# Optimization experiments

Measured on AMD Instinct MI355X. Metric: run time of the kernel, lower is better.

## Reference

```python
import jax, jax.numpy as jnp
import numpy as np

# ---- constant kernels (kornia canny defaults) ----

def _gauss_kernel1d(ksize=5, sigma=1.0):
    x = np.arange(ksize, dtype=np.float32) - (ksize - 1) / 2.0
    g = np.exp(-(x ** 2) / (2.0 * sigma ** 2))
    return (g / g.sum()).astype(np.float32)

_GK = _gauss_kernel1d()
_SOBEL_X = np.array([[-1, 0, 1], [-2, 0, 2], [-1, 0, 1]], np.float32) / 8.0  # normalized=True
_SOBEL_Y = _SOBEL_X.T.copy()

# 8 directional NMS kernels: +1 at center, -1 at neighbor d*45 degrees (kornia order)
_NMS = np.zeros((8, 1, 3, 3), np.float32)
_OFFS = [(0, 1), (1, 1), (1, 0), (1, -1), (0, -1), (-1, -1), (-1, 0), (-1, 1)]
for _i, (_dy, _dx) in enumerate(_OFFS):
    _NMS[_i, 0, 1, 1] = 1.0
    _NMS[_i, 0, 1 + _dy, 1 + _dx] = -1.0


def _conv(x, k):
    return jax.lax.conv_general_dilated(
        x, k, (1, 1), 'VALID', dimension_numbers=('NCHW', 'OIHW', 'NCHW'))


def _canny_dilate(x):
    # x: [B,3,H,W] BGR in [0,1]
    x = x[:, ::-1]  # bgr -> rgb
    gray = 0.299 * x[:, 0:1] + 0.587 * x[:, 1:2] + 0.114 * x[:, 2:3]  # [B,1,H,W]

    # gaussian blur 5x5, sigma=1, reflect padding (separable)
    p = jnp.pad(gray, ((0, 0), (0, 0), (2, 2), (2, 2)), mode='reflect')
    kh = jnp.asarray(_GK).reshape(1, 1, 1, 5)
    kv = jnp.asarray(_GK).reshape(1, 1, 5, 1)
    blurred = _conv(_conv(p, kh), kv)

    # sobel gradients, replicate padding
    sp = jnp.pad(blurred, ((0, 0), (0, 0), (1, 1), (1, 1)), mode='edge')
    sob = jnp.asarray(np.stack([_SOBEL_X, _SOBEL_Y])[:, None])  # (2,1,3,3)
    g = _conv(sp, sob)
    gx, gy = g[:, 0:1], g[:, 1:2]

    mag = jnp.sqrt(gx * gx + gy * gy + 1e-6)  # [B,1,H,W]
    ang45 = jnp.round(jnp.arctan2(gy, gx) * (180.0 / np.pi) / 45.0)  # multiples of 45 deg
    pos_idx = jnp.mod(ang45, 8).astype(jnp.int32)
    neg_idx = jnp.mod(ang45 + 4, 8).astype(jnp.int32)

    # direction-dependent non-maximum suppression
    nms = _conv(jnp.pad(mag, ((0, 0), (0, 0), (1, 1), (1, 1))), jnp.asarray(_NMS))  # [B,8,H,W]
    pos = jnp.take_along_axis(nms, pos_idx, axis=1)
    neg = jnp.take_along_axis(nms, neg_idx, axis=1)
    is_max = jnp.minimum(pos, neg) > 0.0
    mag = mag * is_max

    # morphological dilation, 5x5 ones kernel, geodesic border (pad with -max_val)
    MAX_VAL = 1e4
    padded = jnp.pad(mag, ((0, 0), (0, 0), (2, 2), (2, 2)), constant_values=-MAX_VAL)
    out = jax.lax.reduce_window(padded, -jnp.inf, jax.lax.max,
                                (1, 1, 5, 5), (1, 1, 1, 1), 'VALID')
    return out


def setup_inputs() -> dict:
    key = jax.random.key(0)
    x = jax.random.uniform(key, (32, 3, 512, 512), dtype=jnp.float32)
    return {'x': x}


def reference(x):
    return _canny_dilate(x)
```

## Files before the change

### kernel.cpp

```cpp
#include <hip/hip_runtime.h>
#include <math.h>

#define IMW 512
#define SEG 32
#define NSEG (512/SEG)
#define NSTRIP 10
#define OUTW 52

__device__ __forceinline__ int reflect512(int i) {
    int a = i < 0 ? -i : i;
    int b = 1022 - a;
    return a < b ? a : b;
}
__device__ __forceinline__ float bperm(int a4, float v) {
    return __int_as_float(__builtin_amdgcn_ds_bpermute(a4, __float_as_int(v)));
}

__global__ __launch_bounds__(256)
void canny_pipe(const float* __restrict__ x, float* __restrict__ out) {
    const int lane  = threadIdx.x & 63;
    const int unit  = __builtin_amdgcn_readfirstlane(
                          (int)(blockIdx.x * 4 + (threadIdx.x >> 6)));
    const int img   = unit / (NSTRIP * NSEG);
    const int rem   = unit - img * (NSTRIP * NSEG);
    const int strip = rem / NSEG;
    const int seg   = rem - strip * NSEG;
    const int Y0 = seg * SEG, Y1 = Y0 + SEG;
    const int x0 = strip * OUTW - 6;
    const int xv = x0 + lane;
    const int xr = reflect512(xv);
    const bool inimg  = (xv >= 0) && (xv < IMW);
    const bool stlane = (lane >= 6) && (lane < 58) && (xv < IMW);
    const int l4  = lane << 2;
    const int aL4 = (min(max(xv - 1, 0), 511) - x0) << 2;
    const int aR4 = (min(max(xv + 1, 0), 511) - x0) << 2;

    const float* base = x + (size_t)img * 3 * IMW * IMW;
    const int r0 = reflect512(Y0 - 6);
    const float* b0 = base + (size_t)r0 * IMW;
    const float* b1 = b0 + (size_t)IMW * IMW;
    const float* b2 = b0 + (size_t)2 * IMW * IMW;
    float* ob = out + (size_t)img * IMW * IMW;

    const float K0 = 0.054488684549643f, K1 = 0.244201342003233f, K2 = 0.402619946931554f;

    float hb0=0,hb1=0,hb2=0,hb3=0,hb4=0;
    float hx0=0,hx1=0,hx2=0, hy0=0,hy1=0,hy2=0;
    float mg0=0,mg1=0,mg2=0;
    int   ax0=0, ax1=0;
    float cm0=0,cm1=0,cm2=0,cm3=0,cm4=0;

    float p0 = b0[xr];
    float p1 = b1[xr];
    float p2 = b2[xr];

    #pragma unroll 4
    for (int v = Y0 - 6; v <= Y1 + 5; ++v) {
        float gray = 0.299f * p2 + 0.587f * p1 + 0.114f * p0;
        const int d = ((unsigned)v <= 510u) ? IMW : -IMW;
        b0 += d; b1 += d; b2 += d;
        p0 = b0[xr];
        p1 = b1[xr];
        p2 = b2[xr];

        float gl1 = bperm(l4 - 4, gray), gl2 = bperm(l4 - 8, gray);
        float gr1 = bperm(l4 + 4, gray), gr2 = bperm(l4 + 8, gray);
        hb0 = hb1; hb1 = hb2; hb2 = hb3; hb3 = hb4;
        hb4 = K0 * (gl2 + gr2) + K1 * (gl1 + gr1) + K2 * gray;

        float blur = K0 * (hb0 + hb4) + K1 * (hb1 + hb3) + K2 * hb2;
        float bl = bperm(aL4, blur), br = bperm(aR4, blur);
        hx0 = hx1; hx1 = hx2; hx2 = br - bl;
        hy0 = hy1; hy1 = hy2; hy2 = bl + 2.f * blur + br;

        const int g = v - 3;
        float hxa = (g == 0)   ? hx1 : hx0;
        float hxc = (g == 511) ? hx1 : hx2;
        float hya = (g == 0)   ? hy1 : hy0;
        float hyc = (g == 511) ? hy1 : hy2;
        float gxv = (hxa + 2.f * hx1 + hxc) * 0.125f;
        float gyv = (hyc - hya) * 0.125f;
        float mag = sqrtf(gxv * gxv + gyv * gyv + 1e-6f);
        float axm = fabsf(gxv), aym = fabsf(gyv);
        int axis;
        if (aym <= 0.41421356237309515f * axm)      axis = 0;
        else if (aym >= 2.4142135623730951f * axm)  axis = 2;
        else axis = ((gxv >= 0.f) == (gyv >= 0.f)) ? 1 : 3;
        mg0 = mg1; mg1 = mg2; mg2 = inimg ? mag : 0.f;
        ax0 = ax1; ax1 = axis;

        const int m = v - 4;
        float magm = (m == 0)   ? 0.f : mg0;
        float magc = mg1;
        float magp = (m == 511) ? 0.f : mg2;
        float gcp = bperm(l4 + 4, magc), gcm = bperm(l4 - 4, magc);
        float gpp = bperm(l4 + 4, magp), gpm = bperm(l4 - 4, magp);
        float gmm = bperm(l4 - 4, magm), gmp = bperm(l4 + 4, magm);
        const int dd = ax0;
        float mp = (dd == 0) ? gcp : (dd == 1) ? gpp : (dd == 2) ? magp : gpm;
        float mn = (dd == 0) ? gcm : (dd == 1) ? gmm : (dd == 2) ? magm : gmp;
        float msk = (inimg && fminf(magc - mp, magc - mn) > 0.f) ? magc : 0.f;

        float s1 = fmaxf(bperm(l4 - 4, msk), bperm(l4 + 4, msk));
        float s2 = fmaxf(bperm(l4 - 8, msk), bperm(l4 + 8, msk));
        cm0 = cm1; cm1 = cm2; cm2 = cm3; cm3 = cm4;
        cm4 = fmaxf(fmaxf(s1, s2), msk);

        const int y = v - 6;
        if (y >= Y0) {
            float c0 = (y >= 2)   ? cm0 : 0.f;
            float c1 = (y >= 1)   ? cm1 : 0.f;
            float c3 = (y <= 510) ? cm3 : 0.f;
            float c4 = (y <= 509) ? cm4 : 0.f;
            float val = fmaxf(fmaxf(fmaxf(c0, c1), fmaxf(cm2, c3)), c4);
            if (stlane) ob[(size_t)y * IMW + xv] = val;
        }
    }
}

extern "C" void kernel_launch(void* const* d_in, const int* in_sizes, int n_in,
                              void* d_out, int out_size, void* d_ws, size_t ws_size,
                              hipStream_t stream) {
    const float* x = (const float*)d_in[0];
    float* out = (float*)d_out;
    const int units = 32 * NSTRIP * NSEG;
    dim3 grid(units / 4);
    canny_pipe<<<grid, 256, 0, stream>>>(x, out);
}
```

Before: 175.7 us.

## Process two columns per lane and software-pipeline cross-lane permutes

Each lane now handles two adjacent pixels, so a wavefront covers a 116-column strip instead of 52. This cuts the redundant halo columns and halves the number of ds_bpermute exchanges per pixel. The permute results are staggered across loop iterations, with extra pipeline delay rows, so their latency overlaps with other work. Stores become float2. The cost is more live registers and a longer warm-up per segment.

```diff
diff --git a/kernel.cpp b/kernel.cpp
--- a/kernel.cpp
+++ b/kernel.cpp
@@ -4,8 +4,8 @@
 #define IMW 512
 #define SEG 32
 #define NSEG (512/SEG)
-#define NSTRIP 10
-#define OUTW 52
+#define NSTRIP 5
+#define OUTW 116
 
 __device__ __forceinline__ int reflect512(int i) {
     int a = i < 0 ? -i : i;
@@ -16,104 +16,162 @@
     return __int_as_float(__builtin_amdgcn_ds_bpermute(a4, __float_as_int(v)));
 }
 
-__global__ __launch_bounds__(256)
-void canny_pipe(const float* __restrict__ x, float* __restrict__ out) {
-    const int lane  = threadIdx.x & 63;
-    const int unit  = __builtin_amdgcn_readfirstlane(
-                          (int)(blockIdx.x * 4 + (threadIdx.x >> 6)));
+__global__ __launch_bounds__(128)
+void canny_pipe2(const float* __restrict__ x, float* __restrict__ out) {
+    const int lane = threadIdx.x & 63;
+    const int unit = __builtin_amdgcn_readfirstlane(
+                         (int)(blockIdx.x * 2 + (threadIdx.x >> 6)));
     const int img   = unit / (NSTRIP * NSEG);
     const int rem   = unit - img * (NSTRIP * NSEG);
     const int strip = rem / NSEG;
     const int seg   = rem - strip * NSEG;
     const int Y0 = seg * SEG, Y1 = Y0 + SEG;
-    const int x0 = strip * OUTW - 6;
-    const int xv = x0 + lane;
-    const int xr = reflect512(xv);
-    const bool inimg  = (xv >= 0) && (xv < IMW);
-    const bool stlane = (lane >= 6) && (lane < 58) && (xv < IMW);
-    const int l4  = lane << 2;
-    const int aL4 = (min(max(xv - 1, 0), 511) - x0) << 2;
-    const int aR4 = (min(max(xv + 1, 0), 511) - x0) << 2;
+    const int xbase = strip * OUTW - 6;
+    const int xa = xbase + 2 * lane, xb = xa + 1;
+    const int xra = reflect512(xa), xrb = reflect512(xb);
+    const bool inA = (xa >= 0) && (xa < IMW);
+    const bool inB = (xb >= 0) && (xb < IMW);
+    const bool stl = (lane >= 3) && (lane < 61) && (xb < IMW);
+    const int lm4 = ((lane - 1) & 63) << 2;
+    const int lp4 = ((lane + 1) & 63) << 2;
+    const bool clampL = (xa == 0);
+    const bool clampR = (xb == IMW - 1);
 
     const float* base = x + (size_t)img * 3 * IMW * IMW;
-    const int r0 = reflect512(Y0 - 6);
-    const float* b0 = base + (size_t)r0 * IMW;
+    const float* b0 = base + (size_t)reflect512(Y0 - 6) * IMW;
     const float* b1 = b0 + (size_t)IMW * IMW;
     const float* b2 = b0 + (size_t)2 * IMW * IMW;
     float* ob = out + (size_t)img * IMW * IMW;
 
     const float K0 = 0.054488684549643f, K1 = 0.244201342003233f, K2 = 0.402619946931554f;
 
-    float hb0=0,hb1=0,hb2=0,hb3=0,hb4=0;
-    float hx0=0,hx1=0,hx2=0, hy0=0,hy1=0,hy2=0;
-    float mg0=0,mg1=0,mg2=0;
-    int   ax0=0, ax1=0;
-    float cm0=0,cm1=0,cm2=0,cm3=0,cm4=0;
+    float h0a=0,h1a=0,h2a=0,h3a=0,h4a=0, h0b=0,h1b=0,h2b=0,h3b=0,h4b=0;
+    float hxA0=0,hxA1=0,hxA2=0, hxB0=0,hxB1=0,hxB2=0;
+    float hyA0=0,hyA1=0,hyA2=0, hyB0=0,hyB1=0,hyB2=0;
+    float mgA0=0,mgA1=0,mgA2=0, mgB0=0,mgB1=0,mgB2=0;
+    float smM0=0,smM1=0,smM2=0, smP0=0,smP1=0,smP2=0;
+    int   axA0=0,axA1=0,axA2=0, axB0=0,axB1=0,axB2=0;
+    float cmA0=0,cmA1=0,cmA2=0,cmA3=0,cmA4=0;
+    float cmB0=0,cmB1=0,cmB2=0,cmB3=0,cmB4=0;
+    float pga=0, pgb=0;
+    float pba=0, pbb=0;
+    float psa=0, psb=0;
+    float qg_am=0, qg_ap=0, qg_bm=0, qg_bp=0;
+    float qb_bm=0, qb_ap=0;
+    float qm_bm=0, qm_ap=0;
+    float qs_am=0, qs_ap=0, qs_bm=0, qs_bp=0;
 
-    float p0 = b0[xr];
-    float p1 = b1[xr];
-    float p2 = b2[xr];
+    float f0a = b0[xra], f0b = b0[xrb];
+    float f1a = b1[xra], f1b = b1[xrb];
+    float f2a = b2[xra], f2b = b2[xrb];
 
     #pragma unroll 4
-    for (int v = Y0 - 6; v <= Y1 + 5; ++v) {
-        float gray = 0.299f * p2 + 0.587f * p1 + 0.114f * p0;
+    for (int v = Y0 - 6; v <= Y1 + 9; ++v) {
+        float ga = 0.299f * f2a + 0.587f * f1a + 0.114f * f0a;
+        float gb = 0.299f * f2b + 0.587f * f1b + 0.114f * f0b;
         const int d = ((unsigned)v <= 510u) ? IMW : -IMW;
         b0 += d; b1 += d; b2 += d;
-        p0 = b0[xr];
-        p1 = b1[xr];
-        p2 = b2[xr];
+        f0a = b0[xra]; f0b = b0[xrb];
+        f1a = b1[xra]; f1b = b1[xrb];
+        f2a = b2[xra]; f2b = b2[xrb];
 
-        float gl1 = bperm(l4 - 4, gray), gl2 = bperm(l4 - 8, gray);
-        float gr1 = bperm(l4 + 4, gray), gr2 = bperm(l4 + 8, gray);
-        hb0 = hb1; hb1 = hb2; hb2 = hb3; hb3 = hb4;
-        hb4 = K0 * (gl2 + gr2) + K1 * (gl1 + gr1) + K2 * gray;
+        float hba = K0 * (qg_am + qg_ap) + K1 * (qg_bm + pgb) + K2 * pga;
+        float hbb = K0 * (qg_bm + qg_bp) + K1 * (pga + qg_ap) + K2 * pgb;
+        pga = ga; pgb = gb;
+        qg_am = bperm(lm4, ga); qg_ap = bperm(lp4, ga);
+        qg_bm = bperm(lm4, gb); qg_bp = bperm(lp4, gb);
+        h0a=h1a; h1a=h2a; h2a=h3a; h3a=h4a; h4a=hba;
+        h0b=h1b; h1b=h2b; h2b=h3b; h3b=h4b; h4b=hbb;
 
-        float blur = K0 * (hb0 + hb4) + K1 * (hb1 + hb3) + K2 * hb2;
-        float bl = bperm(aL4, blur), br = bperm(aR4, blur);
-        hx0 = hx1; hx1 = hx2; hx2 = br - bl;
-        hy0 = hy1; hy1 = hy2; hy2 = bl + 2.f * blur + br;
+        float bla = K0 * (h0a + h4a) + K1 * (h1a + h3a) + K2 * h2a;
+        float blb = K0 * (h0b + h4b) + K1 * (h1b + h3b) + K2 * h2b;
 
-        const int g = v - 3;
-        float hxa = (g == 0)   ? hx1 : hx0;
-        float hxc = (g == 511) ? hx1 : hx2;
-        float hya = (g == 0)   ? hy1 : hy0;
-        float hyc = (g == 511) ? hy1 : hy2;
-        float gxv = (hxa + 2.f * hx1 + hxc) * 0.125f;
-        float gyv = (hyc - hya) * 0.125f;
-        float mag = sqrtf(gxv * gxv + gyv * gyv + 1e-6f);
-        float axm = fabsf(gxv), aym = fabsf(gyv);
-        int axis;
-        if (aym <= 0.41421356237309515f * axm)      axis = 0;
-        else if (aym >= 2.4142135623730951f * axm)  axis = 2;
-        else axis = ((gxv >= 0.f) == (gyv >= 0.f)) ? 1 : 3;
-        mg0 = mg1; mg1 = mg2; mg2 = inimg ? mag : 0.f;
-        ax0 = ax1; ax1 = axis;
+        smM0=smM1; smM1=smM2; smM2=qm_bm;
+        smP0=smP1; smP1=smP2; smP2=qm_ap;
+        {
+            const int m = v - 7;
+            float m0a = (m==0)?0.f:mgA0, m0b = (m==0)?0.f:mgB0;
+            float s0m = (m==0)?0.f:smM0, s0p = (m==0)?0.f:smP0;
+            float m2a = (m==511)?0.f:mgA2, m2b = (m==511)?0.f:mgB2;
+            float s2m = (m==511)?0.f:smM2, s2p = (m==511)?0.f:smP2;
+            const int da = axA1;
+            float mpa = (da==0) ? mgB1 : (da==1) ? m2b : (da==2) ? m2a : s2m;
+            float mna = (da==0) ? smM1 : (da==1) ? s0m : (da==2) ? m0a : m0b;
+            float cena = mgA1;
+            float mska_ = (inA && fminf(cena - mpa, cena - mna) > 0.f) ? cena : 0.f;
+            const int db = axB1;
+            float mpb = (db==0) ? smP1 : (db==1) ? s2p : (db==2) ? m2b : m2a;
+            float mnb = (db==0) ? mgA1 : (db==1) ? m0a : (db==2) ? m0b : s0p;
+            float cenb = mgB1;
+            float mskb_ = (inB && fminf(cenb - mpb, cenb - mnb) > 0.f) ? cenb : 0.f;
 
-        const int m = v - 4;
-        float magm = (m == 0)   ? 0.f : mg0;
-        float magc = mg1;
-        float magp = (m == 511) ? 0.f : mg2;
-        float gcp = bperm(l4 + 4, magc), gcm = bperm(l4 - 4, magc);
-        float gpp = bperm(l4 + 4, magp), gpm = bperm(l4 - 4, magp);
-        float gmm = bperm(l4 - 4, magm), gmp = bperm(l4 + 4, magm);
-        const int dd = ax0;
-        float mp = (dd == 0) ? gcp : (dd == 1) ? gpp : (dd == 2) ? magp : gpm;
-        float mn = (dd == 0) ? gcm : (dd == 1) ? gmm : (dd == 2) ? magm : gmp;
-        float msk = (inimg && fminf(magc - mp, magc - mn) > 0.f) ? magc : 0.f;
+            float cma = fmaxf(fmaxf(qs_am, qs_bm), fmaxf(fmaxf(psa, psb), qs_ap));
+            float cmb = fmaxf(fmaxf(qs_bm, psa), fmaxf(fmaxf(psb, qs_ap), qs_bp));
+            cmA0=cmA1; cmA1=cmA2; cmA2=cmA3; cmA3=cmA4; cmA4=cma;
+            cmB0=cmB1; cmB1=cmB2; cmB2=cmB3; cmB3=cmB4; cmB4=cmb;
+            psa = mska_; psb = mskb_;
+            qs_am = bperm(lm4, mska_); qs_ap = bperm(lp4, mska_);
+            qs_bm = bperm(lm4, mskb_); qs_bp = bperm(lp4, mskb_);
+        }
 
-        float s1 = fmaxf(bperm(l4 - 4, msk), bperm(l4 + 4, msk));
-        float s2 = fmaxf(bperm(l4 - 8, msk), bperm(l4 + 8, msk));
-        cm0 = cm1; cm1 = cm2; cm2 = cm3; cm3 = cm4;
-        cm4 = fmaxf(fmaxf(s1, s2), msk);
+        {
+            float la = clampL ? pba : qb_bm;
+            float ra = pbb;
+            float lb = pba;
+            float rb = clampR ? pbb : qb_ap;
+            float nxa = ra - la, nya = la + 2.f * pba + ra;
+            float nxb = rb - lb, nyb = lb + 2.f * pbb + rb;
+            hxA0=hxA1; hxA1=hxA2; hxA2=nxa;  hxB0=hxB1; hxB1=hxB2; hxB2=nxb;
+            hyA0=hyA1; hyA1=hyA2; hyA2=nya;  hyB0=hyB1; hyB1=hyB2; hyB2=nyb;
+            pba = bla; pbb = blb;
+            qb_bm = bperm(lm4, blb); qb_ap = bperm(lp4, bla);
+        }
 
-        const int y = v - 6;
-        if (y >= Y0) {
-            float c0 = (y >= 2)   ? cm0 : 0.f;
-            float c1 = (y >= 1)   ? cm1 : 0.f;
-            float c3 = (y <= 510) ? cm3 : 0.f;
-            float c4 = (y <= 509) ? cm4 : 0.f;
-            float val = fmaxf(fmaxf(fmaxf(c0, c1), fmaxf(cm2, c3)), c4);
-            if (stlane) ob[(size_t)y * IMW + xv] = val;
+        {
+            const int g = v - 5;
+            float hxaa = (g==0) ? hxA1 : hxA0;  float hxca = (g==511) ? hxA1 : hxA2;
+            float hyaa = (g==0) ? hyA1 : hyA0;  float hyca = (g==511) ? hyA1 : hyA2;
+            float gxa = (hxaa + 2.f * hxA1 + hxca) * 0.125f;
+            float gya = (hyca - hyaa) * 0.125f;
+            float maga = sqrtf(gxa * gxa + gya * gya + 1e-6f);
+            float axma = fabsf(gxa), ayma = fabsf(gya);
+            int aa;
+            if (ayma <= 0.41421356237309515f * axma)      aa = 0;
+            else if (ayma >= 2.4142135623730951f * axma)  aa = 2;
+            else aa = ((gxa >= 0.f) == (gya >= 0.f)) ? 1 : 3;
+
+            float hxab = (g==0) ? hxB1 : hxB0;  float hxcb = (g==511) ? hxB1 : hxB2;
+            float hyab = (g==0) ? hyB1 : hyB0;  float hycb = (g==511) ? hyB1 : hyB2;
+            float gxb = (hxab + 2.f * hxB1 + hxcb) * 0.125f;
+            float gyb = (hycb - hyab) * 0.125f;
+            float magb = sqrtf(gxb * gxb + gyb * gyb + 1e-6f);
+            float axmb = fabsf(gxb), aymb = fabsf(gyb);
+            int ab;
+            if (aymb <= 0.41421356237309515f * axmb)      ab = 0;
+            else if (aymb >= 2.4142135623730951f * axmb)  ab = 2;
+            else ab = ((gxb >= 0.f) == (gyb >= 0.f)) ? 1 : 3;
+
+            mgA0=mgA1; mgA1=mgA2; mgA2 = inA ? maga : 0.f;
+            mgB0=mgB1; mgB1=mgB2; mgB2 = inB ? magb : 0.f;
+            axA0=axA1; axA1=axA2; axA2=aa;
+            axB0=axB1; axB1=axB2; axB2=ab;
+            qm_bm = bperm(lm4, mgB2); qm_ap = bperm(lp4, mgA2);
+        }
+
+        {
+            const int y = v - 10;
+            if (y >= Y0) {
+                float c0a=(y>=2)?cmA0:0.f, c1a=(y>=1)?cmA1:0.f;
+                float c3a=(y<=510)?cmA3:0.f, c4a=(y<=509)?cmA4:0.f;
+                float va = fmaxf(fmaxf(fmaxf(c0a, c1a), fmaxf(cmA2, c3a)), c4a);
+                float c0b=(y>=2)?cmB0:0.f, c1b=(y>=1)?cmB1:0.f;
+                float c3b=(y<=510)?cmB3:0.f, c4b=(y<=509)?cmB4:0.f;
+                float vb = fmaxf(fmaxf(fmaxf(c0b, c1b), fmaxf(cmB2, c3b)), c4b);
+                if (stl) {
+                    float2 t; t.x = va; t.y = vb;
+                    *(float2*)(ob + (size_t)y * IMW + xa) = t;
+                }
+            }
         }
     }
 }
@@ -124,6 +182,6 @@
     const float* x = (const float*)d_in[0];
     float* out = (float*)d_out;
     const int units = 32 * NSTRIP * NSEG;
-    dim3 grid(units / 4);
-    canny_pipe<<<grid, 256, 0, stream>>>(x, out);
+    dim3 grid(units / 2);
+    canny_pipe2<<<grid, 128, 0, stream>>>(x, out);
 }
```

After: 179.4 us. 2.1% more time.

## Process full image rows per wavefront with 8 pixels per lane and DPP shuffles

Applied to the files above, without the earlier changes.

Replaces the 64-wide overlapping column strips (52 useful lanes of 64) with one wavefront covering an entire 512-pixel row, where each lane holds 8 pixels loaded as two float4 vectors. Horizontal neighbour exchange moves from ds_bpermute to DPP row rotates and shifts plus in-register access, and the segment height drops from 32 to 8 rows. Interior segments use a template specialization with no border checks, and the block index is swizzled. This removes the redundant strip-overlap work and the LDS-permute traffic, but the short segments mean 12 warm-up rows per 8 output rows, which adds recomputation and raises register pressure.

```diff
diff --git a/kernel.cpp b/kernel.cpp
--- a/kernel.cpp
+++ b/kernel.cpp
@@ -2,120 +2,303 @@
 #include <math.h>
 
 #define IMW 512
-#define SEG 32
-#define NSEG (512/SEG)
-#define NSTRIP 10
-#define OUTW 52
+#define SEG 8
+#define NSEG 64
+
+template<int CTRL>
+__device__ __forceinline__ float dpp_mov(float v) {
+    return __int_as_float(__builtin_amdgcn_update_dpp(
+        0, __float_as_int(v), CTRL, 0xF, 0xF, true));
+}
+#define ROTR1(v) dpp_mov<0x13C>(v)
+#define SHR1(v)  dpp_mov<0x138>(v)
+#define ROTL1(v) dpp_mov<0x134>(v)
+#define SHL1(v)  dpp_mov<0x130>(v)
 
 __device__ __forceinline__ int reflect512(int i) {
     int a = i < 0 ? -i : i;
     int b = 1022 - a;
     return a < b ? a : b;
 }
-__device__ __forceinline__ float bperm(int a4, float v) {
-    return __int_as_float(__builtin_amdgcn_ds_bpermute(a4, __float_as_int(v)));
-}
-
-__global__ __launch_bounds__(256)
-void canny_pipe(const float* __restrict__ x, float* __restrict__ out) {
-    const int lane  = threadIdx.x & 63;
-    const int unit  = __builtin_amdgcn_readfirstlane(
-                          (int)(blockIdx.x * 4 + (threadIdx.x >> 6)));
-    const int img   = unit / (NSTRIP * NSEG);
-    const int rem   = unit - img * (NSTRIP * NSEG);
-    const int strip = rem / NSEG;
-    const int seg   = rem - strip * NSEG;
+
+struct CT { static constexpr bool value = true;  };
+struct CF { static constexpr bool value = false; };
+
+template<bool EDGE>
+__device__ __forceinline__ void run_rows(
+    const float* b0, const float* b1, const float* b2, float* ob,
+    const int Y0, const int Y1, const int lane)
+{
+    const float K0 = 0.054488684549643f, K1 = 0.244201342003233f,
+                K2 = 0.402619946931554f;
+    const bool l0  = (lane == 0);
+    const bool l63 = (lane == 63);
+    const int  vo  = lane * 4;
+
+    float hb[5][8];
+    float hx[3][8], hy[3][8];
+    float mg[3][8];
+    int   ax[2][8];
+    float cm[5][8];
+    #pragma unroll
+    for (int r = 0; r < 5; ++r) {
+        #pragma unroll
+        for (int e = 0; e < 8; ++e) { hb[r][e] = 0.f; cm[r][e] = 0.f; }
+    }
+    #pragma unroll
+    for (int r = 0; r < 3; ++r) {
+        #pragma unroll
+        for (int e = 0; e < 8; ++e) { hx[r][e] = 0.f; hy[r][e] = 0.f; mg[r][e] = 0.f; }
+    }
+    #pragma unroll
+    for (int r = 0; r < 2; ++r) {
+        #pragma unroll
+        for (int e = 0; e < 8; ++e) ax[r][e] = 0;
+    }
+
+    float4 c0A = *(const float4*)(b0 + vo), c0B = *(const float4*)(b0 + 256 + vo);
+    float4 c1A = *(const float4*)(b1 + vo), c1B = *(const float4*)(b1 + 256 + vo);
+    float4 c2A = *(const float4*)(b2 + vo), c2B = *(const float4*)(b2 + 256 + vo);
+
+    auto iter = [&](int v, auto st) {
+        constexpr bool STORE = decltype(st)::value;
+
+        float gA[4] = {
+            0.299f*c2A.x + 0.587f*c1A.x + 0.114f*c0A.x,
+            0.299f*c2A.y + 0.587f*c1A.y + 0.114f*c0A.y,
+            0.299f*c2A.z + 0.587f*c1A.z + 0.114f*c0A.z,
+            0.299f*c2A.w + 0.587f*c1A.w + 0.114f*c0A.w };
+        float gB[4] = {
+            0.299f*c2B.x + 0.587f*c1B.x + 0.114f*c0B.x,
+            0.299f*c2B.y + 0.587f*c1B.y + 0.114f*c0B.y,
+            0.299f*c2B.z + 0.587f*c1B.z + 0.114f*c0B.z,
+            0.299f*c2B.w + 0.587f*c1B.w + 0.114f*c0B.w };
+
+        {
+            int d;
+            if constexpr (EDGE) d = ((unsigned)v <= 510u) ? IMW : -IMW;
+            else                d = IMW;
+            b0 += d; b1 += d; b2 += d;
+        }
+        c0A = *(const float4*)(b0 + vo); c0B = *(const float4*)(b0 + 256 + vo);
+        c1A = *(const float4*)(b1 + vo); c1B = *(const float4*)(b1 + 256 + vo);
+        c2A = *(const float4*)(b2 + vo); c2B = *(const float4*)(b2 + 256 + vo);
+
+        {
+            float rAe2 = ROTR1(gA[2]), rAe3 = ROTR1(gA[3]);
+            float rBe2 = ROTR1(gB[2]), rBe3 = ROTR1(gB[3]);
+            float lAe0 = ROTL1(gA[0]), lAe1 = ROTL1(gA[1]);
+            float lBe0 = ROTL1(gB[0]), lBe1 = ROTL1(gB[1]);
+            float Am1 = l0  ? gA[1] : rAe3;
+            float Am2 = l0  ? gA[2] : rAe2;
+            float Bm1 = l0  ? rAe3  : rBe3;
+            float Bm2 = l0  ? rAe2  : rBe2;
+            float Ap1 = l63 ? lBe0  : lAe0;
+            float Ap2 = l63 ? lBe1  : lAe1;
+            float Bp1 = l63 ? gB[2] : lBe0;
+            float Bp2 = l63 ? gB[1] : lBe1;
+            float nh[8] = {
+                K0*(Am2  +gA[2]) + K1*(Am1  +gA[1]) + K2*gA[0],
+                K0*(Am1  +gA[3]) + K1*(gA[0]+gA[2]) + K2*gA[1],
+                K0*(gA[0]+Ap1  ) + K1*(gA[1]+gA[3]) + K2*gA[2],
+                K0*(gA[1]+Ap2  ) + K1*(gA[2]+Ap1  ) + K2*gA[3],
+                K0*(Bm2  +gB[2]) + K1*(Bm1  +gB[1]) + K2*gB[0],
+                K0*(Bm1  +gB[3]) + K1*(gB[0]+gB[2]) + K2*gB[1],
+                K0*(gB[0]+Bp1  ) + K1*(gB[1]+gB[3]) + K2*gB[2],
+                K0*(gB[1]+Bp2  ) + K1*(gB[2]+Bp1  ) + K2*gB[3] };
+            #pragma unroll
+            for (int r = 0; r < 4; ++r) {
+                #pragma unroll
+                for (int e = 0; e < 8; ++e) hb[r][e] = hb[r+1][e];
+            }
+            #pragma unroll
+            for (int e = 0; e < 8; ++e) hb[4][e] = nh[e];
+        }
+
+        {
+            float bl[8];
+            #pragma unroll
+            for (int e = 0; e < 8; ++e)
+                bl[e] = K0*(hb[0][e]+hb[4][e]) + K1*(hb[1][e]+hb[3][e]) + K2*hb[2][e];
+            float rA3 = ROTR1(bl[3]), rB3 = ROTR1(bl[7]);
+            float lA0 = ROTL1(bl[0]), lB0 = ROTL1(bl[4]);
+            float sAm1 = l0  ? bl[0] : rA3;
+            float sBm1 = l0  ? rA3   : rB3;
+            float sAp1 = l63 ? lB0   : lA0;
+            float sBp1 = l63 ? bl[7] : lB0;
+            float nx[8] = { bl[1]-sAm1, bl[2]-bl[0], bl[3]-bl[1], sAp1-bl[2],
+                            bl[5]-sBm1, bl[6]-bl[4], bl[7]-bl[5], sBp1-bl[6] };
+            float ny[8] = { sAm1+2.f*bl[0]+bl[1], bl[0]+2.f*bl[1]+bl[2],
+                            bl[1]+2.f*bl[2]+bl[3], bl[2]+2.f*bl[3]+sAp1,
+                            sBm1+2.f*bl[4]+bl[5], bl[4]+2.f*bl[5]+bl[6],
+                            bl[5]+2.f*bl[6]+bl[7], bl[6]+2.f*bl[7]+sBp1 };
+            #pragma unroll
+            for (int r = 0; r < 2; ++r) {
+                #pragma unroll
+                for (int e = 0; e < 8; ++e) { hx[r][e] = hx[r+1][e]; hy[r][e] = hy[r+1][e]; }
+            }
+            #pragma unroll
+            for (int e = 0; e < 8; ++e) { hx[2][e] = nx[e]; hy[2][e] = ny[e]; }
+        }
+
+        {
+            const int g = v - 3;
+            float nmg[8]; int nax[8];
+            #pragma unroll
+            for (int e = 0; e < 8; ++e) {
+                float hxa, hxc, hya, hyc;
+                if constexpr (EDGE) {
+                    hxa = (g==0)   ? hx[1][e] : hx[0][e];
+                    hxc = (g==511) ? hx[1][e] : hx[2][e];
+                    hya = (g==0)   ? hy[1][e] : hy[0][e];
+                    hyc = (g==511) ? hy[1][e] : hy[2][e];
+                } else {
+                    hxa = hx[0][e]; hxc = hx[2][e]; hya = hy[0][e]; hyc = hy[2][e];
+                }
+                float gx = (hxa + 2.f*hx[1][e] + hxc) * 0.125f;
+                float gy = (hyc - hya) * 0.125f;
+                float mag = sqrtf(gx*gx + gy*gy + 1e-6f);
+                float axm = fabsf(gx), aym = fabsf(gy);
+                int a;
+                if (aym <= 0.41421356237309515f * axm)      a = 0;
+                else if (aym >= 2.4142135623730951f * axm)  a = 2;
+                else a = ((gx >= 0.f) == (gy >= 0.f)) ? 1 : 3;
+                nmg[e] = mag; nax[e] = a;
+            }
+            #pragma unroll
+            for (int r = 0; r < 2; ++r) {
+                #pragma unroll
+                for (int e = 0; e < 8; ++e) mg[r][e] = mg[r+1][e];
+            }
+            #pragma unroll
+            for (int e = 0; e < 8; ++e) { mg[2][e] = nmg[e]; ax[0][e] = ax[1][e]; ax[1][e] = nax[e]; }
+        }
+
+        {
+            float M0[8], M2[8];
+            if constexpr (EDGE) {
+                const int m = v - 4;
+                #pragma unroll
+                for (int e = 0; e < 8; ++e) {
+                    M0[e] = (m==0)   ? 0.f : mg[0][e];
+                    M2[e] = (m==511) ? 0.f : mg[2][e];
+                }
+            } else {
+                #pragma unroll
+                for (int e = 0; e < 8; ++e) { M0[e] = mg[0][e]; M2[e] = mg[2][e]; }
+            }
+            float M0l[8], M0r[8], M1l[8], M1r[8], M2l[8], M2r[8];
+            auto make_ins = [&](const float* R, float* Lv, float* Rv) {
+                float ra3 = ROTR1(R[3]), rb3 = ROTR1(R[7]);
+                float la0 = ROTL1(R[0]), lb0 = ROTL1(R[4]);
+                float shA = SHR1(R[3]);
+                float shB = SHL1(R[4]);
+                float mB  = l0  ? ra3 : rb3;
+                float pA  = l63 ? lb0 : la0;
+                Lv[0]=shA;  Lv[1]=R[0]; Lv[2]=R[1]; Lv[3]=R[2];
+                Lv[4]=mB;   Lv[5]=R[4]; Lv[6]=R[5]; Lv[7]=R[6];
+                Rv[0]=R[1]; Rv[1]=R[2]; Rv[2]=R[3]; Rv[3]=pA;
+                Rv[4]=R[5]; Rv[5]=R[6]; Rv[6]=R[7]; Rv[7]=shB;
+            };
+            make_ins(M0,    M0l, M0r);
+            make_ins(mg[1], M1l, M1r);
+            make_ins(M2,    M2l, M2r);
+
+            float msk[8];
+            #pragma unroll
+            for (int e = 0; e < 8; ++e) {
+                const int d = ax[0][e];
+                float c  = mg[1][e];
+                float mp = (d==0) ? M1r[e] : (d==1) ? M2r[e] : (d==2) ? M2[e] : M2l[e];
+                float mn = (d==0) ? M1l[e] : (d==1) ? M0l[e] : (d==2) ? M0[e] : M0r[e];
+                msk[e] = (fminf(c - mp, c - mn) > 0.f) ? c : 0.f;
+            }
+
+            float cr2 = ROTR1(msk[2]), cr3 = ROTR1(msk[3]);
+            float dr2 = ROTR1(msk[6]), dr3 = ROTR1(msk[7]);
+            float el0 = ROTL1(msk[0]), el1 = ROTL1(msk[1]);
+            float fl0 = ROTL1(msk[4]), fl1 = ROTL1(msk[5]);
+            float sA2 = SHR1(msk[2]),  sA3 = SHR1(msk[3]);
+            float tB0 = SHL1(msk[4]),  tB1 = SHL1(msk[5]);
+            float Am2 = sA2, Am1 = sA3;
+            float Bm2 = l0  ? cr2 : dr2, Bm1 = l0  ? cr3 : dr3;
+            float Ap1 = l63 ? fl0 : el0, Ap2 = l63 ? fl1 : el1;
+            float Bp1 = tB0, Bp2 = tB1;
+            float ncm[8] = {
+                fmaxf(fmaxf(fmaxf(Am1,    msk[1]), fmaxf(Am2,    msk[2])), msk[0]),
+                fmaxf(fmaxf(fmaxf(msk[0], msk[2]), fmaxf(Am1,    msk[3])), msk[1]),
+                fmaxf(fmaxf(fmaxf(msk[1], msk[3]), fmaxf(msk[0], Ap1   )), msk[2]),
+                fmaxf(fmaxf(fmaxf(msk[2], Ap1   ), fmaxf(msk[1], Ap2   )), msk[3]),
+                fmaxf(fmaxf(fmaxf(Bm1,    msk[5]), fmaxf(Bm2,    msk[6])), msk[4]),
+                fmaxf(fmaxf(fmaxf(msk[4], msk[6]), fmaxf(Bm1,    msk[7])), msk[5]),
+                fmaxf(fmaxf(fmaxf(msk[5], msk[7]), fmaxf(msk[4], Bp1   )), msk[6]),
+                fmaxf(fmaxf(fmaxf(msk[6], Bp1   ), fmaxf(msk[5], Bp2   )), msk[7]) };
+            #pragma unroll
+            for (int r = 0; r < 4; ++r) {
+                #pragma unroll
+                for (int e = 0; e < 8; ++e) cm[r][e] = cm[r+1][e];
+            }
+            #pragma unroll
+            for (int e = 0; e < 8; ++e) cm[4][e] = ncm[e];
+        }
+
+        if constexpr (STORE) {
+            const int y = v - 6;
+            bool go = true;
+            if constexpr (EDGE) go = (y >= Y0);
+            if (go) {
+                float o[8];
+                #pragma unroll
+                for (int e = 0; e < 8; ++e) {
+                    float c0 = cm[0][e], c1 = cm[1][e], c3 = cm[3][e], c4 = cm[4][e];
+                    if constexpr (EDGE) {
+                        c0 = (y>=2)   ? c0 : 0.f;
+                        c1 = (y>=1)   ? c1 : 0.f;
+                        c3 = (y<=510) ? c3 : 0.f;
+                        c4 = (y<=509) ? c4 : 0.f;
+                    }
+                    o[e] = fmaxf(fmaxf(fmaxf(c0, c1), fmaxf(cm[2][e], c3)), c4);
+                }
+                float* orow = ob + (size_t)y * IMW;
+                float4 t0; t0.x=o[0]; t0.y=o[1]; t0.z=o[2]; t0.w=o[3];
+                float4 t1; t1.x=o[4]; t1.y=o[5]; t1.z=o[6]; t1.w=o[7];
+                *(float4*)(orow + vo)       = t0;
+                *(float4*)(orow + 256 + vo) = t1;
+            }
+        }
+    };
+
+    if constexpr (EDGE) {
+        #pragma unroll 2
+        for (int v = Y0 - 6; v < Y1 + 6; ++v) iter(v, CT{});
+    } else {
+        #pragma unroll 4
+        for (int v = Y0 - 6; v < Y0 + 6; ++v) iter(v, CF{});
+        #pragma unroll 4
+        for (int v = Y0 + 6; v < Y1 + 6; ++v) iter(v, CT{});
+    }
+}
+
+__global__ __launch_bounds__(256, 2)
+void canny_row(const float* __restrict__ x, float* __restrict__ out) {
+    const int lane = threadIdx.x & 63;
+    const int b = blockIdx.x;
+    const int l = ((b & 7) << 6) + (b >> 3);
+    const int unit = __builtin_amdgcn_readfirstlane(l * 4 + (int)(threadIdx.x >> 6));
+    const int img = unit >> 6;
+    const int seg = unit & 63;
     const int Y0 = seg * SEG, Y1 = Y0 + SEG;
-    const int x0 = strip * OUTW - 6;
-    const int xv = x0 + lane;
-    const int xr = reflect512(xv);
-    const bool inimg  = (xv >= 0) && (xv < IMW);
-    const bool stlane = (lane >= 6) && (lane < 58) && (xv < IMW);
-    const int l4  = lane << 2;
-    const int aL4 = (min(max(xv - 1, 0), 511) - x0) << 2;
-    const int aR4 = (min(max(xv + 1, 0), 511) - x0) << 2;
 
     const float* base = x + (size_t)img * 3 * IMW * IMW;
-    const int r0 = reflect512(Y0 - 6);
-    const float* b0 = base + (size_t)r0 * IMW;
+    const float* b0 = base + (size_t)reflect512(Y0 - 6) * IMW;
     const float* b1 = b0 + (size_t)IMW * IMW;
     const float* b2 = b0 + (size_t)2 * IMW * IMW;
     float* ob = out + (size_t)img * IMW * IMW;
 
-    const float K0 = 0.054488684549643f, K1 = 0.244201342003233f, K2 = 0.402619946931554f;
-
-    float hb0=0,hb1=0,hb2=0,hb3=0,hb4=0;
-    float hx0=0,hx1=0,hx2=0, hy0=0,hy1=0,hy2=0;
-    float mg0=0,mg1=0,mg2=0;
-    int   ax0=0, ax1=0;
-    float cm0=0,cm1=0,cm2=0,cm3=0,cm4=0;
-
-    float p0 = b0[xr];
-    float p1 = b1[xr];
-    float p2 = b2[xr];
-
-    #pragma unroll 4
-    for (int v = Y0 - 6; v <= Y1 + 5; ++v) {
-        float gray = 0.299f * p2 + 0.587f * p1 + 0.114f * p0;
-        const int d = ((unsigned)v <= 510u) ? IMW : -IMW;
-        b0 += d; b1 += d; b2 += d;
-        p0 = b0[xr];
-        p1 = b1[xr];
-        p2 = b2[xr];
-
-        float gl1 = bperm(l4 - 4, gray), gl2 = bperm(l4 - 8, gray);
-        float gr1 = bperm(l4 + 4, gray), gr2 = bperm(l4 + 8, gray);
-        hb0 = hb1; hb1 = hb2; hb2 = hb3; hb3 = hb4;
-        hb4 = K0 * (gl2 + gr2) + K1 * (gl1 + gr1) + K2 * gray;
-
-        float blur = K0 * (hb0 + hb4) + K1 * (hb1 + hb3) + K2 * hb2;
-        float bl = bperm(aL4, blur), br = bperm(aR4, blur);
-        hx0 = hx1; hx1 = hx2; hx2 = br - bl;
-        hy0 = hy1; hy1 = hy2; hy2 = bl + 2.f * blur + br;
-
-        const int g = v - 3;
-        float hxa = (g == 0)   ? hx1 : hx0;
-        float hxc = (g == 511) ? hx1 : hx2;
-        float hya = (g == 0)   ? hy1 : hy0;
-        float hyc = (g == 511) ? hy1 : hy2;
-        float gxv = (hxa + 2.f * hx1 + hxc) * 0.125f;
-        float gyv = (hyc - hya) * 0.125f;
-        float mag = sqrtf(gxv * gxv + gyv * gyv + 1e-6f);
-        float axm = fabsf(gxv), aym = fabsf(gyv);
-        int axis;
-        if (aym <= 0.41421356237309515f * axm)      axis = 0;
-        else if (aym >= 2.4142135623730951f * axm)  axis = 2;
-        else axis = ((gxv >= 0.f) == (gyv >= 0.f)) ? 1 : 3;
-        mg0 = mg1; mg1 = mg2; mg2 = inimg ? mag : 0.f;
-        ax0 = ax1; ax1 = axis;
-
-        const int m = v - 4;
-        float magm = (m == 0)   ? 0.f : mg0;
-        float magc = mg1;
-        float magp = (m == 511) ? 0.f : mg2;
-        float gcp = bperm(l4 + 4, magc), gcm = bperm(l4 - 4, magc);
-        float gpp = bperm(l4 + 4, magp), gpm = bperm(l4 - 4, magp);
-        float gmm = bperm(l4 - 4, magm), gmp = bperm(l4 + 4, magm);
-        const int dd = ax0;
-        float mp = (dd == 0) ? gcp : (dd == 1) ? gpp : (dd == 2) ? magp : gpm;
-        float mn = (dd == 0) ? gcm : (dd == 1) ? gmm : (dd == 2) ? magm : gmp;
-        float msk = (inimg && fminf(magc - mp, magc - mn) > 0.f) ? magc : 0.f;
-
-        float s1 = fmaxf(bperm(l4 - 4, msk), bperm(l4 + 4, msk));
-        float s2 = fmaxf(bperm(l4 - 8, msk), bperm(l4 + 8, msk));
-        cm0 = cm1; cm1 = cm2; cm2 = cm3; cm3 = cm4;
-        cm4 = fmaxf(fmaxf(s1, s2), msk);
-
-        const int y = v - 6;
-        if (y >= Y0) {
-            float c0 = (y >= 2)   ? cm0 : 0.f;
-            float c1 = (y >= 1)   ? cm1 : 0.f;
-            float c3 = (y <= 510) ? cm3 : 0.f;
-            float c4 = (y <= 509) ? cm4 : 0.f;
-            float val = fmaxf(fmaxf(fmaxf(c0, c1), fmaxf(cm2, c3)), c4);
-            if (stlane) ob[(size_t)y * IMW + xv] = val;
-        }
-    }
+    if (seg == 0 || seg == NSEG - 1)
+        run_rows<true >(b0, b1, b2, ob, Y0, Y1, lane);
+    else
+        run_rows<false>(b0, b1, b2, ob, Y0, Y1, lane);
 }
 
 extern "C" void kernel_launch(void* const* d_in, const int* in_sizes, int n_in,
@@ -123,7 +306,7 @@
                               hipStream_t stream) {
     const float* x = (const float*)d_in[0];
     float* out = (float*)d_out;
-    const int units = 32 * NSTRIP * NSEG;
+    const int units = 32 * NSEG;
     dim3 grid(units / 4);
-    canny_pipe<<<grid, 256, 0, stream>>>(x, out);
-}
+    canny_row<<<grid, 256, 0, stream>>>(x, out);
+}
```

After: 189.6 us. +7.9%, slower.
